# Performance work log

Measured on AMD Instinct MI355X. Metric: run time of the kernel, lower is better.

## Reference

```python
import jax, jax.numpy as jnp
import numpy as np


def setup_inputs() -> dict:
    key = jax.random.key(0)
    k1, k2, k3 = jax.random.split(key, 3)
    B, DIM, H, Wd = 32, 512, 64, 64
    K, DQ = 64, 3
    features = jax.random.normal(k1, (B, DIM, H, Wd), dtype=jnp.float32)
    query = jax.random.normal(k2, (B, DQ, H, Wd), dtype=jnp.float32)
    # Ensemble of K 1x1 convs (no bias): weight [K, dim_query, dim], scaled like conv init
    W = jax.random.normal(k3, (K, DQ, DIM), dtype=jnp.float32) * (1.0 / np.sqrt(DIM))
    return {"features": features, "query": query, "W": W}


def reference(features, query, W):
    B = query.shape[0]
    # ensemble 1x1 conv: key_values [k, b, q, h, w]
    kv = jnp.einsum('kqd,bdhw->kbqhw', W, features)
    # rearrange 'k b ... -> b k ...'
    kv_b = jnp.transpose(kv, (1, 0, 2, 3, 4))          # [b, k, q, h, w]
    q_flat = query.reshape(B, 1, -1)                    # [b, 1, N]
    kv_flat = kv_b.reshape(B, kv_b.shape[1], -1)        # [b, k, N]
    # torch.cdist (p=2) between [b,1,N] and [b,k,N] -> [b,k]
    diff = q_flat - kv_flat
    distance = jnp.sqrt(jnp.sum(diff * diff, axis=-1))  # [b, k]
    codes = jnp.argmin(distance, axis=-1)               # [b]
    # batched gather of selected key_values
    idx = codes[:, None, None, None, None]
    sel_key_values = jnp.take_along_axis(kv_b, idx, axis=1)[:, 0]  # [b, q, h, w]
    commit_loss = jnp.mean((sel_key_values - query) ** 2)
    return sel_key_values, codes, commit_loss
```

## Files before the change

### kernel.cpp

```cpp
#include <hip/hip_runtime.h>
#include <hip/hip_bf16.h>
#include <hip/hip_fp16.h>

#define BN   32
#define DIMK 512
#define HW   4096
#define KK   64
#define DQ   3
#define RR   192
#define NT   64
#define NBLK (HW / NT)

typedef _Float16 half8 __attribute__((ext_vector_type(8)));
typedef float    f32x4 __attribute__((ext_vector_type(4)));

#define A16_OFF    0
#define A16_BYTES  (RR * DIMK * 2)
#define DIST2_OFF  196608
#define DIST2_BYTES (BN * KK * 4)
#define LOSSB_OFF  (DIST2_OFF + DIST2_BYTES)
#define KV_OFF     262144
#define KV_BYTES   ((size_t)BN * RR * HW * 2)

__global__ void init_kernel(const float* __restrict__ Wsrc,
                            _Float16* __restrict__ A16,
                            float* __restrict__ dist2,
                            float* __restrict__ lossb) {
  int gid = blockIdx.x * 256 + threadIdx.x;
  if (gid < RR * DIMK) A16[gid] = (_Float16)Wsrc[gid];
  if (gid < BN * KK)   dist2[gid] = 0.f;
  if (gid < BN)        lossb[gid] = 0.f;
}

template <bool STORE>
__global__ __launch_bounds__(256) void gemm_dist_kernel(
    const float* __restrict__ f, const float* __restrict__ query,
    const _Float16* __restrict__ A16, __hip_bfloat16* __restrict__ kv,
    float* __restrict__ dist2) {
  __shared__ __align__(16) _Float16 Alds[RR][40];
  __shared__ __align__(16) _Float16 Blds[4][NT][8];
  __shared__ float qlds[DQ][NT];
  __shared__ float rowsum[RR];

  const int t  = threadIdx.x;
  const int w  = t >> 6;
  const int l  = t & 63;
  const int lq = l >> 4;
  const int ln = l & 15;
  const int b  = blockIdx.y;
  const int n0 = blockIdx.x * NT;

  if (t < DQ * NT) {
    int q = t / NT, n = t % NT;
    qlds[q][n] = query[((size_t)b * DQ + q) * HW + n0 + n];
  }

  f32x4 acc[3][4];
#pragma unroll
  for (int mt = 0; mt < 3; mt++)
#pragma unroll
    for (int nt = 0; nt < 4; nt++) acc[mt][nt] = (f32x4)0.f;

  const int bn  = t & 63;
  const int bkb = t >> 6;

  for (int kk = 0; kk < DIMK / 32; kk++) {
    const int dbase = kk * 32;
    __syncthreads();
#pragma unroll
    for (int i = 0; i < 3; i++) {
      int s = t + i * 256;
      int m = s >> 2, oct = s & 3;
      half8 av = *(const half8*)&A16[m * DIMK + dbase + oct * 8];
      *(half8*)&Alds[m][oct * 8] = av;
    }
    {
      const float* fp = f + ((size_t)b * DIMK + dbase + bkb * 8) * HW + n0 + bn;
      float v[8];
#pragma unroll
      for (int j = 0; j < 8; j++) v[j] = fp[(size_t)j * HW];
      half8 hv;
#pragma unroll
      for (int j = 0; j < 8; j++) hv[j] = (_Float16)v[j];
      *(half8*)&Blds[bkb][bn][0] = hv;
    }
    __syncthreads();

    half8 af[3], bf[4];
#pragma unroll
    for (int mt = 0; mt < 3; mt++)
      af[mt] = *(const half8*)&Alds[w * 48 + mt * 16 + ln][lq * 8];
#pragma unroll
    for (int nt = 0; nt < 4; nt++)
      bf[nt] = *(const half8*)&Blds[lq][nt * 16 + ln][0];
#pragma unroll
    for (int mt = 0; mt < 3; mt++)
#pragma unroll
      for (int nt = 0; nt < 4; nt++)
        acc[mt][nt] = __builtin_amdgcn_mfma_f32_16x16x32_f16(af[mt], bf[nt],
                                                             acc[mt][nt], 0, 0, 0);
  }

  float rs[3][4];
#pragma unroll
  for (int mt = 0; mt < 3; mt++)
#pragma unroll
    for (int i = 0; i < 4; i++) rs[mt][i] = 0.f;

#pragma unroll
  for (int mt = 0; mt < 3; mt++) {
#pragma unroll
    for (int i = 0; i < 4; i++) {
      int r = w * 48 + mt * 16 + lq * 4 + i;
      int q = r % 3;
#pragma unroll
      for (int nt = 0; nt < 4; nt++) {
        int n = nt * 16 + ln;
        float c = acc[mt][nt][i];
        if (STORE) kv[((size_t)b * RR + r) * HW + n0 + n] = __float2bfloat16(c);
        float d = c - qlds[q][n];
        rs[mt][i] += d * d;
      }
    }
  }
#pragma unroll
  for (int mt = 0; mt < 3; mt++)
#pragma unroll
    for (int i = 0; i < 4; i++) {
      float v = rs[mt][i];
      v += __shfl_xor(v, 1, 64);
      v += __shfl_xor(v, 2, 64);
      v += __shfl_xor(v, 4, 64);
      v += __shfl_xor(v, 8, 64);
      rs[mt][i] = v;
    }
  if (ln < 12) {
    int mt = ln >> 2, i = ln & 3;
    rowsum[w * 48 + mt * 16 + lq * 4 + i] = rs[mt][i];
  }
  __syncthreads();
  if (t < KK) {
    float v = rowsum[3 * t] + rowsum[3 * t + 1] + rowsum[3 * t + 2];
    atomicAdd(&dist2[b * KK + t], v);
  }
}

__global__ __launch_bounds__(256) void gather_kernel(
    const __hip_bfloat16* __restrict__ kv, const float* __restrict__ query,
    const float* __restrict__ dist2, float* __restrict__ out,
    float* __restrict__ lossb) {
  int b = blockIdx.x, t = threadIdx.x;
  __shared__ int scode;
  __shared__ float red[4];
  if (t == 0) {
    float best = dist2[b * KK]; int bi = 0;
    for (int k = 1; k < KK; k++) {
      float v = dist2[b * KK + k];
      if (v < best) { best = v; bi = k; }
    }
    scode = bi;
    out[(size_t)BN * DQ * HW + b] = (float)bi;
  }
  __syncthreads();
  int code = scode;
  const __hip_bfloat16* src = kv + ((size_t)b * RR + code * DQ) * HW;
  const float* qp = query + (size_t)b * DQ * HW;
  float* op = out + (size_t)b * DQ * HW;
  float lsum = 0.f;
  for (int idx = t; idx < DQ * HW; idx += 256) {
    float v = __bfloat162float(src[idx]);
    op[idx] = v;
    float d = v - qp[idx];
    lsum += d * d;
  }
  for (int off = 1; off < 64; off <<= 1) lsum += __shfl_xor(lsum, off, 64);
  if ((t & 63) == 0) red[t >> 6] = lsum;
  __syncthreads();
  if (t == 0) lossb[b] = red[0] + red[1] + red[2] + red[3];
}

__global__ __launch_bounds__(256) void recompute_kernel(
    const float* __restrict__ f, const float* __restrict__ query,
    const float* __restrict__ Wsrc, const float* __restrict__ dist2,
    float* __restrict__ out, float* __restrict__ lossb) {
  int b = blockIdx.y, t = threadIdx.x;
  int hw = blockIdx.x * 256 + t;
  __shared__ int scode;
  __shared__ float red[4];
  if (t == 0) {
    float best = dist2[b * KK]; int bi = 0;
    for (int k = 1; k < KK; k++) {
      float v = dist2[b * KK + k];
      if (v < best) { best = v; bi = k; }
    }
    scode = bi;
    if (blockIdx.x == 0) out[(size_t)BN * DQ * HW + b] = (float)bi;
  }
  __syncthreads();
  int code = scode;
  const float* w0 = Wsrc + (size_t)code * DQ * DIMK;
  const float* fp = f + (size_t)b * DIMK * HW + hw;
  float a0 = 0.f, a1 = 0.f, a2 = 0.f;
  for (int d = 0; d < DIMK; d++) {
    float fv = fp[(size_t)d * HW];
    a0 += w0[d] * fv;
    a1 += w0[DIMK + d] * fv;
    a2 += w0[2 * DIMK + d] * fv;
  }
  const float* qp = query + (size_t)b * DQ * HW;
  float* op = out + (size_t)b * DQ * HW;
  op[hw] = a0; op[HW + hw] = a1; op[2 * HW + hw] = a2;
  float d0 = a0 - qp[hw], d1 = a1 - qp[HW + hw], d2 = a2 - qp[2 * HW + hw];
  float lsum = d0 * d0 + d1 * d1 + d2 * d2;
  for (int off = 1; off < 64; off <<= 1) lsum += __shfl_xor(lsum, off, 64);
  if ((t & 63) == 0) red[t >> 6] = lsum;
  __syncthreads();
  if (t == 0) atomicAdd(&lossb[b], red[0] + red[1] + red[2] + red[3]);
}

__global__ void finalize_kernel(const float* __restrict__ lossb,
                                float* __restrict__ out) {
  if (threadIdx.x == 0) {
    float s = 0.f;
    for (int b = 0; b < BN; b++) s += lossb[b];
    out[(size_t)BN * DQ * HW + BN] = s / (float)(BN * DQ * HW);
  }
}

extern "C" void kernel_launch(void* const* d_in, const int* in_sizes, int n_in,
                              void* d_out, int out_size, void* d_ws, size_t ws_size,
                              hipStream_t stream) {
  const float* f     = (const float*)d_in[0];
  const float* query = (const float*)d_in[1];
  const float* Wsrc  = (const float*)d_in[2];
  float* out = (float*)d_out;
  char*  ws  = (char*)d_ws;

  _Float16*        A16   = (_Float16*)(ws + A16_OFF);
  float*           dist2 = (float*)(ws + DIST2_OFF);
  float*           lossb = (float*)(ws + LOSSB_OFF);
  __hip_bfloat16*  kv    = (__hip_bfloat16*)(ws + KV_OFF);

  const bool store = ws_size >= (size_t)KV_OFF + KV_BYTES;

  init_kernel<<<384, 256, 0, stream>>>(Wsrc, A16, dist2, lossb);
  if (store) {
    gemm_dist_kernel<true><<<dim3(NBLK, BN), 256, 0, stream>>>(f, query, A16, kv, dist2);
    gather_kernel<<<BN, 256, 0, stream>>>(kv, query, dist2, out, lossb);
  } else {
    gemm_dist_kernel<false><<<dim3(NBLK, BN), 256, 0, stream>>>(f, query, A16, nullptr, dist2);
    recompute_kernel<<<dim3(HW / 256, BN), 256, 0, stream>>>(f, query, Wsrc, dist2, out, lossb);
  }
  finalize_kernel<<<1, 64, 0, stream>>>(lossb, out);
}
```

Measured before the change: 417.5 us.

## Double-buffer GEMM tiles, widen N tile, vectorize gather, drop finalize kernel

The GEMM kernel now uses double-buffered LDS with register prefetch of the next K-slice, so global loads overlap the MFMA work on the current slice. The N tile doubles to 128, which halves how often the weight matrix is reloaded per column and doubles accumulators per wave. The gather kernel switches to 128-bit vector loads and stores with manual bf16-to-float conversion. The per-batch loss buffer and finalize kernel are replaced by a scaled atomicAdd into the output, removing one launch. The costs are higher register and LDS use, which may lower occupancy, and a grid of half as many blocks.

```diff
diff --git a/kernel.cpp b/kernel.cpp
--- a/kernel.cpp
+++ b/kernel.cpp
@@ -8,28 +8,31 @@
 #define KK   64
 #define DQ   3
 #define RR   192
-#define NT   64
+#define NT   128
 #define NBLK (HW / NT)
 
-typedef _Float16 half8 __attribute__((ext_vector_type(8)));
-typedef float    f32x4 __attribute__((ext_vector_type(4)));
+typedef _Float16 half8  __attribute__((ext_vector_type(8)));
+typedef float    f32x4  __attribute__((ext_vector_type(4)));
+typedef short    short8 __attribute__((ext_vector_type(8)));
 
 #define A16_OFF    0
 #define A16_BYTES  (RR * DIMK * 2)
 #define DIST2_OFF  196608
 #define DIST2_BYTES (BN * KK * 4)
-#define LOSSB_OFF  (DIST2_OFF + DIST2_BYTES)
 #define KV_OFF     262144
 #define KV_BYTES   ((size_t)BN * RR * HW * 2)
+
+#define OUT_SEL    ((size_t)BN * DQ * HW)
+#define OUT_LOSS   (OUT_SEL + BN)
 
 __global__ void init_kernel(const float* __restrict__ Wsrc,
                             _Float16* __restrict__ A16,
                             float* __restrict__ dist2,
-                            float* __restrict__ lossb) {
+                            float* __restrict__ out) {
   int gid = blockIdx.x * 256 + threadIdx.x;
   if (gid < RR * DIMK) A16[gid] = (_Float16)Wsrc[gid];
   if (gid < BN * KK)   dist2[gid] = 0.f;
-  if (gid < BN)        lossb[gid] = 0.f;
+  if (gid == 0)        out[OUT_LOSS] = 0.f;
 }
 
 template <bool STORE>
@@ -37,8 +40,8 @@
     const float* __restrict__ f, const float* __restrict__ query,
     const _Float16* __restrict__ A16, __hip_bfloat16* __restrict__ kv,
     float* __restrict__ dist2) {
-  __shared__ __align__(16) _Float16 Alds[RR][40];
-  __shared__ __align__(16) _Float16 Blds[4][NT][8];
+  __shared__ __align__(16) _Float16 Alds[2][RR][40];
+  __shared__ __align__(16) _Float16 Blds[2][4][NT][8];
   __shared__ float qlds[DQ][NT];
   __shared__ float rowsum[RR];
 
@@ -50,55 +53,69 @@
   const int b  = blockIdx.y;
   const int n0 = blockIdx.x * NT;
 
-  if (t < DQ * NT) {
-    int q = t / NT, n = t % NT;
+  for (int s = t; s < DQ * NT; s += 256) {
+    int q = s / NT, n = s % NT;
     qlds[q][n] = query[((size_t)b * DQ + q) * HW + n0 + n];
   }
 
-  f32x4 acc[3][4];
+  f32x4 acc[3][8];
 #pragma unroll
   for (int mt = 0; mt < 3; mt++)
 #pragma unroll
-    for (int nt = 0; nt < 4; nt++) acc[mt][nt] = (f32x4)0.f;
-
-  const int bn  = t & 63;
-  const int bkb = t >> 6;
-
-  for (int kk = 0; kk < DIMK / 32; kk++) {
-    const int dbase = kk * 32;
-    __syncthreads();
+    for (int nt = 0; nt < 8; nt++) acc[mt][nt] = (f32x4)0.f;
+
+  const int bn  = t & (NT - 1);
+  const int bkb = t >> 7;
+
+  float bpre[16];
+  half8 apre[3];
+
+  auto loadTile = [&](int kk) {
+    const float* fp = f + ((size_t)b * DIMK + kk * 32 + bkb * 16) * HW + n0 + bn;
+#pragma unroll
+    for (int j = 0; j < 16; j++) bpre[j] = fp[(size_t)j * HW];
 #pragma unroll
     for (int i = 0; i < 3; i++) {
       int s = t + i * 256;
       int m = s >> 2, oct = s & 3;
-      half8 av = *(const half8*)&A16[m * DIMK + dbase + oct * 8];
-      *(half8*)&Alds[m][oct * 8] = av;
-    }
-    {
-      const float* fp = f + ((size_t)b * DIMK + dbase + bkb * 8) * HW + n0 + bn;
-      float v[8];
-#pragma unroll
-      for (int j = 0; j < 8; j++) v[j] = fp[(size_t)j * HW];
-      half8 hv;
-#pragma unroll
-      for (int j = 0; j < 8; j++) hv[j] = (_Float16)v[j];
-      *(half8*)&Blds[bkb][bn][0] = hv;
-    }
+      apre[i] = *(const half8*)&A16[m * DIMK + kk * 32 + oct * 8];
+    }
+  };
+  auto stageTile = [&](int buf) {
+#pragma unroll
+    for (int i = 0; i < 3; i++) {
+      int s = t + i * 256;
+      int m = s >> 2, oct = s & 3;
+      *(half8*)&Alds[buf][m][oct * 8] = apre[i];
+    }
+    half8 h0, h1;
+#pragma unroll
+    for (int j = 0; j < 8; j++) { h0[j] = (_Float16)bpre[j]; h1[j] = (_Float16)bpre[8 + j]; }
+    *(half8*)&Blds[buf][2 * bkb][bn][0]     = h0;
+    *(half8*)&Blds[buf][2 * bkb + 1][bn][0] = h1;
+  };
+
+  loadTile(0);
+  stageTile(0);
+  for (int kk = 0; kk < DIMK / 32; kk++) {
+    const int cur = kk & 1;
     __syncthreads();
-
-    half8 af[3], bf[4];
+    if (kk < DIMK / 32 - 1) loadTile(kk + 1);
+
+    half8 af[3], bf[8];
 #pragma unroll
     for (int mt = 0; mt < 3; mt++)
-      af[mt] = *(const half8*)&Alds[w * 48 + mt * 16 + ln][lq * 8];
-#pragma unroll
-    for (int nt = 0; nt < 4; nt++)
-      bf[nt] = *(const half8*)&Blds[lq][nt * 16 + ln][0];
+      af[mt] = *(const half8*)&Alds[cur][w * 48 + mt * 16 + ln][lq * 8];
+#pragma unroll
+    for (int nt = 0; nt < 8; nt++)
+      bf[nt] = *(const half8*)&Blds[cur][lq][nt * 16 + ln][0];
 #pragma unroll
     for (int mt = 0; mt < 3; mt++)
 #pragma unroll
-      for (int nt = 0; nt < 4; nt++)
+      for (int nt = 0; nt < 8; nt++)
         acc[mt][nt] = __builtin_amdgcn_mfma_f32_16x16x32_f16(af[mt], bf[nt],
                                                              acc[mt][nt], 0, 0, 0);
+    if (kk < DIMK / 32 - 1) stageTile(cur ^ 1);
   }
 
   float rs[3][4];
@@ -114,7 +131,7 @@
       int r = w * 48 + mt * 16 + lq * 4 + i;
       int q = r % 3;
 #pragma unroll
-      for (int nt = 0; nt < 4; nt++) {
+      for (int nt = 0; nt < 8; nt++) {
         int n = nt * 16 + ln;
         float c = acc[mt][nt][i];
         if (STORE) kv[((size_t)b * RR + r) * HW + n0 + n] = __float2bfloat16(c);
@@ -147,8 +164,7 @@
 
 __global__ __launch_bounds__(256) void gather_kernel(
     const __hip_bfloat16* __restrict__ kv, const float* __restrict__ query,
-    const float* __restrict__ dist2, float* __restrict__ out,
-    float* __restrict__ lossb) {
+    const float* __restrict__ dist2, float* __restrict__ out) {
   int b = blockIdx.x, t = threadIdx.x;
   __shared__ int scode;
   __shared__ float red[4];
@@ -159,30 +175,44 @@
       if (v < best) { best = v; bi = k; }
     }
     scode = bi;
-    out[(size_t)BN * DQ * HW + b] = (float)bi;
+    out[OUT_SEL + b] = (float)bi;
   }
   __syncthreads();
   int code = scode;
-  const __hip_bfloat16* src = kv + ((size_t)b * RR + code * DQ) * HW;
-  const float* qp = query + (size_t)b * DQ * HW;
-  float* op = out + (size_t)b * DQ * HW;
+  const short8* src = (const short8*)(kv + ((size_t)b * RR + code * DQ) * HW);
+  const f32x4*  qp  = (const f32x4*)(query + (size_t)b * DQ * HW);
+  f32x4*        op  = (f32x4*)(out + (size_t)b * DQ * HW);
   float lsum = 0.f;
-  for (int idx = t; idx < DQ * HW; idx += 256) {
-    float v = __bfloat162float(src[idx]);
-    op[idx] = v;
-    float d = v - qp[idx];
-    lsum += d * d;
+  for (int c = t; c < DQ * HW / 8; c += 256) {
+    short8 v = src[c];
+    f32x4 o0, o1;
+#pragma unroll
+    for (int j = 0; j < 4; j++) {
+      unsigned u0 = ((unsigned)(unsigned short)v[j]) << 16;
+      unsigned u1 = ((unsigned)(unsigned short)v[4 + j]) << 16;
+      o0[j] = __builtin_bit_cast(float, u0);
+      o1[j] = __builtin_bit_cast(float, u1);
+    }
+    f32x4 q0 = qp[2 * c], q1 = qp[2 * c + 1];
+    op[2 * c] = o0; op[2 * c + 1] = o1;
+#pragma unroll
+    for (int j = 0; j < 4; j++) {
+      float d0 = o0[j] - q0[j], d1 = o1[j] - q1[j];
+      lsum += d0 * d0 + d1 * d1;
+    }
   }
   for (int off = 1; off < 64; off <<= 1) lsum += __shfl_xor(lsum, off, 64);
   if ((t & 63) == 0) red[t >> 6] = lsum;
   __syncthreads();
-  if (t == 0) lossb[b] = red[0] + red[1] + red[2] + red[3];
+  if (t == 0)
+    atomicAdd(&out[OUT_LOSS],
+              (red[0] + red[1] + red[2] + red[3]) * (1.f / (float)(BN * DQ * HW)));
 }
 
 __global__ __launch_bounds__(256) void recompute_kernel(
     const float* __restrict__ f, const float* __restrict__ query,
     const float* __restrict__ Wsrc, const float* __restrict__ dist2,
-    float* __restrict__ out, float* __restrict__ lossb) {
+    float* __restrict__ out) {
   int b = blockIdx.y, t = threadIdx.x;
   int hw = blockIdx.x * 256 + t;
   __shared__ int scode;
@@ -194,7 +224,7 @@
       if (v < best) { best = v; bi = k; }
     }
     scode = bi;
-    if (blockIdx.x == 0) out[(size_t)BN * DQ * HW + b] = (float)bi;
+    if (blockIdx.x == 0) out[OUT_SEL + b] = (float)bi;
   }
   __syncthreads();
   int code = scode;
@@ -215,16 +245,9 @@
   for (int off = 1; off < 64; off <<= 1) lsum += __shfl_xor(lsum, off, 64);
   if ((t & 63) == 0) red[t >> 6] = lsum;
   __syncthreads();
-  if (t == 0) atomicAdd(&lossb[b], red[0] + red[1] + red[2] + red[3]);
-}
-
-__global__ void finalize_kernel(const float* __restrict__ lossb,
-                                float* __restrict__ out) {
-  if (threadIdx.x == 0) {
-    float s = 0.f;
-    for (int b = 0; b < BN; b++) s += lossb[b];
-    out[(size_t)BN * DQ * HW + BN] = s / (float)(BN * DQ * HW);
-  }
+  if (t == 0)
+    atomicAdd(&out[OUT_LOSS],
+              (red[0] + red[1] + red[2] + red[3]) * (1.f / (float)(BN * DQ * HW)));
 }
 
 extern "C" void kernel_launch(void* const* d_in, const int* in_sizes, int n_in,
@@ -238,18 +261,16 @@
 
   _Float16*        A16   = (_Float16*)(ws + A16_OFF);
   float*           dist2 = (float*)(ws + DIST2_OFF);
-  float*           lossb = (float*)(ws + LOSSB_OFF);
   __hip_bfloat16*  kv    = (__hip_bfloat16*)(ws + KV_OFF);
 
   const bool store = ws_size >= (size_t)KV_OFF + KV_BYTES;
 
-  init_kernel<<<384, 256, 0, stream>>>(Wsrc, A16, dist2, lossb);
+  init_kernel<<<384, 256, 0, stream>>>(Wsrc, A16, dist2, out);
   if (store) {
     gemm_dist_kernel<true><<<dim3(NBLK, BN), 256, 0, stream>>>(f, query, A16, kv, dist2);
-    gather_kernel<<<BN, 256, 0, stream>>>(kv, query, dist2, out, lossb);
+    gather_kernel<<<BN, 256, 0, stream>>>(kv, query, dist2, out);
   } else {
     gemm_dist_kernel<false><<<dim3(NBLK, BN), 256, 0, stream>>>(f, query, A16, nullptr, dist2);
-    recompute_kernel<<<dim3(HW / 256, BN), 256, 0, stream>>>(f, query, Wsrc, dist2, out, lossb);
-  }
-  finalize_kernel<<<1, 64, 0, stream>>>(lossb, out);
-}
+    recompute_kernel<<<dim3(HW / 256, BN), 256, 0, stream>>>(f, query, Wsrc, dist2, out);
+  }
+}
```

New measurement: 380.5 us. 1.1x faster.
